# Performance work log

Hardware: AMD Instinct MI355X
Metric: run time of the kernel (lower is better)

## Reference

```python
import jax, jax.numpy as jnp
import numpy as np

N, E, G = 50000, 400000, 64
F_IN, HID, HEADS, GF, NCLS = 16, 128, 4, 10, 6


def _init(k, shape, fan):
    return jax.random.normal(k, shape, jnp.float32) * (1.0 / np.sqrt(fan))


def setup_inputs() -> dict:
    key = jax.random.key(0)
    ks = jax.random.split(key, 16)
    x = jax.random.normal(ks[0], (N, F_IN), jnp.float32)
    edge_index = jax.random.randint(ks[1], (2, E), 0, N)
    batch = jnp.sort(jax.random.randint(ks[2], (N,), 0, G))
    graph_feat = jax.random.normal(ks[3], (G, GF), jnp.float32)
    # GATConv 1: in=16 -> heads=4, out=128, concat
    W1 = _init(ks[4], (F_IN, HEADS * HID), F_IN)
    att_src1 = _init(ks[5], (HEADS, HID), HID)
    att_dst1 = _init(ks[6], (HEADS, HID), HID)
    b1 = jnp.zeros((HEADS * HID,), jnp.float32)
    # GATConv 2: in=512 -> heads=1, out=128, mean (concat=False)
    W2 = _init(ks[7], (HEADS * HID, HID), HEADS * HID)
    att_src2 = _init(ks[8], (1, HID), HID)
    att_dst2 = _init(ks[9], (1, HID), HID)
    b2 = jnp.zeros((HID,), jnp.float32)
    # graph_proj MLP 10->32->32
    Wg1 = _init(ks[10], (GF, 32), GF); bg1 = jnp.zeros((32,), jnp.float32)
    Wg2 = _init(ks[11], (32, 32), 32); bg2 = jnp.zeros((32,), jnp.float32)
    # classifier 160->128->6
    Wc1 = _init(ks[12], (HID + 32, 128), HID + 32); bc1 = jnp.zeros((128,), jnp.float32)
    Wc2 = _init(ks[13], (128, NCLS), 128); bc2 = jnp.zeros((NCLS,), jnp.float32)
    return dict(x=x, edge_index=edge_index, batch=batch, graph_feat=graph_feat,
                W1=W1, att_src1=att_src1, att_dst1=att_dst1, b1=b1,
                W2=W2, att_src2=att_src2, att_dst2=att_dst2, b2=b2,
                Wg1=Wg1, bg1=bg1, Wg2=Wg2, bg2=bg2,
                Wc1=Wc1, bc1=bc1, Wc2=Wc2, bc2=bc2)


def gat_layer(x, W, att_src, att_dst, bias, src, dst, n_nodes, heads, out_dim, concat):
    # Linear transform: [N, H, C]
    h = (x @ W).reshape(n_nodes, heads, out_dim)
    a_src = jnp.einsum('nhc,hc->nh', h, att_src)  # [N,H]
    a_dst = jnp.einsum('nhc,hc->nh', h, att_dst)  # [N,H]
    e = jax.nn.leaky_relu(a_src[src] + a_dst[dst], 0.2)  # [Etot,H]
    # segment softmax over edges grouped by dst (self-loops ensure nonempty)
    m = jax.ops.segment_max(e, dst, num_segments=n_nodes)
    ex = jnp.exp(e - m[dst])
    denom = jax.ops.segment_sum(ex, dst, num_segments=n_nodes)
    alpha = ex / denom[dst]  # [Etot,H]
    out = jax.ops.segment_sum(alpha[:, :, None] * h[src], dst, num_segments=n_nodes)  # [N,H,C]
    if concat:
        out = out.reshape(n_nodes, heads * out_dim)
    else:
        out = out.mean(axis=1)
    return out + bias


def reference(x, edge_index, batch, graph_feat,
              W1, att_src1, att_dst1, b1,
              W2, att_src2, att_dst2, b2,
              Wg1, bg1, Wg2, bg2, Wc1, bc1, Wc2, bc2):
    n = x.shape[0]
    loops = jnp.arange(n, dtype=edge_index.dtype)
    src = jnp.concatenate([edge_index[0], loops])
    dst = jnp.concatenate([edge_index[1], loops])
    h = jax.nn.elu(gat_layer(x, W1, att_src1, att_dst1, b1, src, dst, n, HEADS, HID, True))
    h = jax.nn.elu(gat_layer(h, W2, att_src2, att_dst2, b2, src, dst, n, 1, HID, False))
    # global mean pool over graphs
    g = graph_feat.shape[0]
    sums = jax.ops.segment_sum(h, batch, num_segments=g)
    counts = jax.ops.segment_sum(jnp.ones((n, 1), h.dtype), batch, num_segments=g)
    pooled = sums / jnp.maximum(counts, 1.0)
    gf = jax.nn.relu(graph_feat @ Wg1 + bg1) @ Wg2 + bg2
    z = jnp.concatenate([pooled, gf], axis=1)
    z = jax.nn.relu(z @ Wc1 + bc1)
    return z @ Wc2 + bc2
```

## Files before the change

kernel.cpp:

```cpp
#include <hip/hip_runtime.h>
#include <hip/hip_bf16.h>

#define NN 50000
#define EE 400000
#define GG 64
#define CAP 48

typedef unsigned short u16;
typedef unsigned char u8;
typedef long long i64;
typedef __attribute__((ext_vector_type(8))) short bf16x8;
typedef __attribute__((ext_vector_type(4))) float f32x4;
typedef __attribute__((ext_vector_type(2))) float f32x2;

__device__ __forceinline__ float b2f(u16 u) {
    unsigned int x = ((unsigned int)u) << 16;
    return __uint_as_float(x);
}
__device__ __forceinline__ u16 f2b(float f) {
    unsigned int x = __float_as_uint(f);
    unsigned int r = x + 0x7fffu + ((x >> 16) & 1u);
    return (u16)(r >> 16);
}
__device__ __forceinline__ u8 f2fp8(float f) {
    return (u8)(__builtin_amdgcn_cvt_pk_fp8_f32(f, f, 0, false) & 0xFF);
}
__device__ __forceinline__ f32x2 fp8x2_f32(unsigned int v, bool hi) {
    return hi ? __builtin_amdgcn_cvt_pk_f32_fp8(v, true)
              : __builtin_amdgcn_cvt_pk_f32_fp8(v, false);
}
__device__ __forceinline__ float wred_sum(float v) {
    #pragma unroll
    for (int o = 32; o; o >>= 1) v += __shfl_xor(v, o, 64);
    return v;
}
__device__ __forceinline__ float lrelu(float v) { return v > 0.f ? v : 0.2f * v; }

__global__ void k_prep(const int* __restrict__ batch, int* __restrict__ deg,
                       int* __restrict__ col, int* __restrict__ gstart,
                       const float* __restrict__ W1, const float* __restrict__ as1,
                       const float* __restrict__ ad1, u16* __restrict__ W1p,
                       const float* __restrict__ W2, u8* __restrict__ W2p,
                       float* __restrict__ pooled) {
    __shared__ float asw[16][8];
    int b = blockIdx.x, t = threadIdx.x;
    if (b < 196) {
        int n = b * 256 + t;
        if (n < NN) { deg[n] = 1; col[(size_t)n * CAP] = n; }
    } else if (b == 196) {
        if (t <= GG) {
            int lo = 0, hi = NN;
            while (lo < hi) {
                int mid = (lo + hi) >> 1;
                if (batch[mid] < t) lo = mid + 1; else hi = mid;
            }
            gstart[t] = lo;
        }
    } else if (b < 453) {
        int idx = (b - 197) * 256 + t;
        int j = idx & 7;
        int l = (idx >> 3) & 63;
        int ct = idx >> 9;
        int c = ct >> 3, tt = ct & 7;
        int k = c * 32 + (l >> 4) * 8 + j;
        int n = tt * 16 + (l & 15);
        W2p[idx] = f2fp8(W2[k * 128 + n]);
    } else if (b == 453) {
        int pair = t >> 1, half = t & 1;
        int k = pair >> 3, h = pair & 7;
        int hd = h & 3;
        const float* att = (h >= 4) ? ad1 : as1;
        float s = 0.f;
        int c0 = half * 64;
        for (int c = c0; c < c0 + 64; c++)
            s += W1[k * 512 + hd * 128 + c] * att[hd * 128 + c];
        s += __shfl_xor(s, 1, 64);
        if (half == 0) asw[k][h] = s;
        __syncthreads();
        for (int idx = t; idx < 33 * 64 * 8; idx += 256) {
            int j = idx & 7, l = (idx >> 3) & 63, tt = idx >> 9;
            int quad = l >> 4, m = l & 15;
            int k2 = quad * 8 + j;
            float v = 0.f;
            if (k2 < 16) {
                if (tt < 32) v = W1[k2 * 512 + tt * 16 + m];
                else if (m < 8) v = asw[k2][m];
            }
            W1p[idx] = f2b(v);
        }
    } else {
        for (int i = t; i < GG * 128; i += 256) pooled[i] = 0.f;
    }
}

__global__ void k_edges(const int* __restrict__ ei, int* __restrict__ deg,
                        int* __restrict__ col) {
    int e = blockIdx.x * 256 + threadIdx.x;
    if (e < EE) {
        int s = ei[e];
        int d = ei[EE + e];
        int slot = atomicAdd(&deg[d], 1);
        if (slot < CAP) col[(size_t)d * CAP + slot] = s;
    }
}

__global__ __launch_bounds__(256) void k_gemm1(
    const float* __restrict__ x, const u16* __restrict__ W1p,
    u8* __restrict__ h1, float* __restrict__ a_src1, float* __restrict__ a_dst1) {
    int tid = threadIdx.x;
    int wave = tid >> 6, l = tid & 63;
    int quad = l >> 4, m = l & 15;
    int row0 = blockIdx.x * 64 + wave * 16;
    int arow = row0 + m;
    int arow_c = arow < NN ? arow : (NN - 1);
    bf16x8 af;
    if (quad < 2) {
        const float* xp = x + arow_c * 16 + quad * 8;
        float4 x0 = *(const float4*)(xp);
        float4 x1 = *(const float4*)(xp + 4);
        u16 tmp[8] = {f2b(x0.x), f2b(x0.y), f2b(x0.z), f2b(x0.w),
                      f2b(x1.x), f2b(x1.y), f2b(x1.z), f2b(x1.w)};
        af = *(bf16x8*)tmp;
    } else {
        af = (bf16x8){0, 0, 0, 0, 0, 0, 0, 0};
    }
    const u16* bp = W1p + l * 8;
    f32x4 acc[33];
    #pragma unroll
    for (int tt = 0; tt < 33; tt++) acc[tt] = (f32x4){0.f, 0.f, 0.f, 0.f};
    #pragma unroll
    for (int tt = 0; tt < 33; tt++) {
        bf16x8 bf = *(const bf16x8*)(bp + (size_t)tt * 512);
        acc[tt] = __builtin_amdgcn_mfma_f32_16x16x32_bf16(af, bf, acc[tt], 0, 0, 0);
    }
    #pragma unroll
    for (int r = 0; r < 4; r++) {
        int row = row0 + quad * 4 + r;
        if (row >= NN) continue;
        #pragma unroll
        for (int tt = 0; tt < 32; tt++)
            h1[(size_t)row * 512 + tt * 16 + m] = f2fp8(acc[tt][r]);
        float v = acc[32][r];
        if (m < 4) a_src1[row * 4 + m] = v;
        else if (m < 8) a_dst1[row * 4 + (m - 4)] = v;
    }
}

__global__ __launch_bounds__(256) void k_agg1(
    const int* __restrict__ deg, const int* __restrict__ col,
    const float* __restrict__ a_src1, const float* __restrict__ a_dst1,
    const u8* __restrict__ h1, const float* __restrict__ b1,
    u8* __restrict__ h2pre) {
    __shared__ float alphaS[4][64][4];
    int t = threadIdx.x;
    int wave = t >> 6, l = t & 63;
    int n = blockIdx.x * 4 + wave;
    if (n >= NN) return;
    int dg = min(deg[n], CAP);
    int sl = (l < dg) ? col[(size_t)n * CAP + l] : 0;
    float4 ad = *(const float4*)(a_dst1 + n * 4);
    float4 as = *(const float4*)(a_src1 + (size_t)sl * 4);
    float4 e;
    e.x = __expf(lrelu(as.x + ad.x)); e.y = __expf(lrelu(as.y + ad.y));
    e.z = __expf(lrelu(as.z + ad.z)); e.w = __expf(lrelu(as.w + ad.w));
    if (l >= dg) e = (float4){0.f, 0.f, 0.f, 0.f};
    float4 inv;
    inv.x = 1.0f / wred_sum(e.x);
    inv.y = 1.0f / wred_sum(e.y);
    inv.z = 1.0f / wred_sum(e.z);
    inv.w = 1.0f / wred_sum(e.w);
    {
        float4 a4;
        a4.x = e.x * inv.x; a4.y = e.y * inv.y;
        a4.z = e.z * inv.z; a4.w = e.w * inv.w;
        *(float4*)&alphaS[wave][l][0] = a4;
    }
    int h = l >> 4;
    const u8* hb = h1 + l * 8;
    f32x2 acc[4] = {{0.f, 0.f}, {0.f, 0.f}, {0.f, 0.f}, {0.f, 0.f}};
    int iters = (dg + 3) >> 2;
    for (int j = 0; j < iters; j++) {
        int e0 = 4 * j, e1 = 4 * j + 1, e2 = 4 * j + 2, e3 = 4 * j + 3;
        int s0 = __shfl(sl, e0), s1 = __shfl(sl, e1);
        int s2 = __shfl(sl, e2), s3 = __shfl(sl, e3);
        float a0 = alphaS[wave][e0][h], a1 = alphaS[wave][e1][h];
        float a2 = alphaS[wave][e2][h], a3 = alphaS[wave][e3][h];
        uint2 u0 = *(const uint2*)(hb + (size_t)s0 * 512);
        uint2 u1 = *(const uint2*)(hb + (size_t)s1 * 512);
        uint2 u2 = *(const uint2*)(hb + (size_t)s2 * 512);
        uint2 u3 = *(const uint2*)(hb + (size_t)s3 * 512);
        acc[0] += a0 * fp8x2_f32(u0.x, false);
        acc[1] += a0 * fp8x2_f32(u0.x, true);
        acc[2] += a0 * fp8x2_f32(u0.y, false);
        acc[3] += a0 * fp8x2_f32(u0.y, true);
        acc[0] += a1 * fp8x2_f32(u1.x, false);
        acc[1] += a1 * fp8x2_f32(u1.x, true);
        acc[2] += a1 * fp8x2_f32(u1.y, false);
        acc[3] += a1 * fp8x2_f32(u1.y, true);
        acc[0] += a2 * fp8x2_f32(u2.x, false);
        acc[1] += a2 * fp8x2_f32(u2.x, true);
        acc[2] += a2 * fp8x2_f32(u2.y, false);
        acc[3] += a2 * fp8x2_f32(u2.y, true);
        acc[0] += a3 * fp8x2_f32(u3.x, false);
        acc[1] += a3 * fp8x2_f32(u3.x, true);
        acc[2] += a3 * fp8x2_f32(u3.y, false);
        acc[3] += a3 * fp8x2_f32(u3.y, true);
    }
    int ch0 = l * 8;
    float4 bA = *(const float4*)(b1 + ch0);
    float4 bB = *(const float4*)(b1 + ch0 + 4);
    float av[8] = {acc[0].x, acc[0].y, acc[1].x, acc[1].y,
                   acc[2].x, acc[2].y, acc[3].x, acc[3].y};
    float bb[8] = {bA.x, bA.y, bA.z, bA.w, bB.x, bB.y, bB.z, bB.w};
    float v[8];
    #pragma unroll
    for (int k = 0; k < 8; k++) {
        float w = av[k] + bb[k];
        v[k] = w > 0.f ? w : __expf(w) - 1.0f;
    }
    unsigned int d0 = __builtin_amdgcn_cvt_pk_fp8_f32(v[0], v[1], 0, false);
    d0 = __builtin_amdgcn_cvt_pk_fp8_f32(v[2], v[3], d0, true);
    unsigned int d1 = __builtin_amdgcn_cvt_pk_fp8_f32(v[4], v[5], 0, false);
    d1 = __builtin_amdgcn_cvt_pk_fp8_f32(v[6], v[7], d1, true);
    uint2 ov; ov.x = d0; ov.y = d1;
    *(uint2*)(h2pre + (size_t)n * 512 + ch0) = ov;
}

__global__ __launch_bounds__(256) void k_gemm2(
    const u8* __restrict__ h2pre, const u8* __restrict__ W2p,
    const float* __restrict__ as2, const float* __restrict__ ad2,
    u8* __restrict__ hL2, float* __restrict__ a_src2, float* __restrict__ a_dst2) {
    int t = threadIdx.x;
    int wave = t >> 6, l = t & 63;
    int quad = l >> 4, m = l & 15;
    int row0 = blockIdx.x * 64 + wave * 16;
    int arow = row0 + m;
    int arow_c = arow < NN ? arow : (NN - 1);
    const u8* aptr = h2pre + (size_t)arow_c * 512 + quad * 8;
    const u8* bptr = W2p + l * 8;
    f32x4 acc[8];
    #pragma unroll
    for (int tt = 0; tt < 8; tt++) acc[tt] = (f32x4){0.f, 0.f, 0.f, 0.f};
    for (int c = 0; c < 16; c++) {
        i64 af = *(const i64*)(aptr + c * 32);
        #pragma unroll
        for (int tt = 0; tt < 8; tt++) {
            i64 bf = *(const i64*)(bptr + (size_t)(c * 8 + tt) * 512);
            acc[tt] = __builtin_amdgcn_mfma_f32_16x16x32_fp8_fp8(af, bf, acc[tt], 0, 0, 0);
        }
    }
    float asv[8], adv[8];
    #pragma unroll
    for (int tt = 0; tt < 8; tt++) {
        int colc = tt * 16 + m;
        asv[tt] = as2[colc];
        adv[tt] = ad2[colc];
    }
    #pragma unroll
    for (int r = 0; r < 4; r++) {
        int row = row0 + quad * 4 + r;
        bool ok = row < NN;
        float rs = 0.f, rd = 0.f;
        #pragma unroll
        for (int tt = 0; tt < 8; tt++) {
            float v = acc[tt][r];
            if (ok) hL2[(size_t)row * 128 + tt * 16 + m] = f2fp8(v);
            rs += v * asv[tt];
            rd += v * adv[tt];
        }
        #pragma unroll
        for (int o = 1; o < 16; o <<= 1) {
            rs += __shfl_xor(rs, o, 64);
            rd += __shfl_xor(rd, o, 64);
        }
        if (ok && m == 0) { a_src2[row] = rs; a_dst2[row] = rd; }
    }
}

__global__ __launch_bounds__(256) void k_agg2(
    const int* __restrict__ deg, const int* __restrict__ col,
    const float* __restrict__ a_src2, const float* __restrict__ a_dst2,
    const u8* __restrict__ hL2, const float* __restrict__ b2v,
    const int* __restrict__ batch, float* __restrict__ pooled) {
    __shared__ float red[4][128];
    __shared__ int gS[4];
    int t = threadIdx.x;
    int wave = t >> 6, l = t & 63;
    int n = blockIdx.x * 4 + wave;
    if (n >= NN) return;
    int dg = min(deg[n], CAP);
    int sl = (l < dg) ? col[(size_t)n * CAP + l] : 0;
    float ad = a_dst2[n];
    float e = (l < dg) ? __expf(lrelu(a_src2[sl] + ad)) : 0.f;
    float inv = 1.0f / wred_sum(e);
    float al = e * inv;
    f32x2 acc = {0.f, 0.f};
    const u8* hb = hL2 + l * 2;
    int iters = (dg + 3) >> 2;
    for (int j = 0; j < iters; j++) {
        int e0 = 4 * j, e1 = 4 * j + 1, e2 = 4 * j + 2, e3 = 4 * j + 3;
        int s0 = __shfl(sl, e0), s1 = __shfl(sl, e1);
        int s2 = __shfl(sl, e2), s3 = __shfl(sl, e3);
        float a0 = __shfl(al, e0), a1 = __shfl(al, e1);
        float a2 = __shfl(al, e2), a3 = __shfl(al, e3);
        unsigned int u0 = *(const u16*)(hb + (size_t)s0 * 128);
        unsigned int u1 = *(const u16*)(hb + (size_t)s1 * 128);
        unsigned int u2 = *(const u16*)(hb + (size_t)s2 * 128);
        unsigned int u3 = *(const u16*)(hb + (size_t)s3 * 128);
        acc += a0 * fp8x2_f32(u0, false);
        acc += a1 * fp8x2_f32(u1, false);
        acc += a2 * fp8x2_f32(u2, false);
        acc += a3 * fp8x2_f32(u3, false);
    }
    float o0 = acc.x + b2v[2 * l];     o0 = o0 > 0.f ? o0 : __expf(o0) - 1.0f;
    float o1 = acc.y + b2v[2 * l + 1]; o1 = o1 > 0.f ? o1 : __expf(o1) - 1.0f;
    red[wave][2 * l] = o0;
    red[wave][2 * l + 1] = o1;
    if (l == 0) gS[wave] = batch[n];
    __syncthreads();
    if (t < 128) {
        int g0 = gS[0];
        if (gS[1] == g0 && gS[2] == g0 && gS[3] == g0) {
            float s = red[0][t] + red[1][t] + red[2][t] + red[3][t];
            atomicAdd(&pooled[g0 * 128 + t], s);
        } else {
            #pragma unroll
            for (int w = 0; w < 4; w++)
                atomicAdd(&pooled[gS[w] * 128 + t], red[w][t]);
        }
    }
}

__global__ __launch_bounds__(128) void k_head(
    const int* __restrict__ gstart, const float* __restrict__ pooled,
    const float* __restrict__ gfeat,
    const float* __restrict__ Wg1, const float* __restrict__ bg1,
    const float* __restrict__ Wg2, const float* __restrict__ bg2,
    const float* __restrict__ Wc1, const float* __restrict__ bc1,
    const float* __restrict__ Wc2, const float* __restrict__ bc2,
    float* __restrict__ out) {
    __shared__ float z[160];
    __shared__ float hg[32];
    __shared__ float c1b[128];
    int g = blockIdx.x, t = threadIdx.x;
    float cntf = (float)(gstart[g + 1] - gstart[g]);
    z[t] = pooled[g * 128 + t] / fmaxf(cntf, 1.0f);
    if (t < 32) {
        float a = bg1[t];
        for (int i = 0; i < 10; i++) a += gfeat[g * 10 + i] * Wg1[i * 32 + t];
        hg[t] = fmaxf(a, 0.f);
    }
    __syncthreads();
    if (t < 32) {
        float a = bg2[t];
        for (int i = 0; i < 32; i++) a += hg[i] * Wg2[i * 32 + t];
        z[128 + t] = a;
    }
    __syncthreads();
    float a = bc1[t];
    for (int i = 0; i < 160; i++) a += z[i] * Wc1[i * 128 + t];
    c1b[t] = fmaxf(a, 0.f);
    __syncthreads();
    if (t < 6) {
        float o = bc2[t];
        for (int i = 0; i < 128; i++) o += c1b[i] * Wc2[i * 6 + t];
        out[g * 6 + t] = o;
    }
}

extern "C" void kernel_launch(void* const* d_in, const int* in_sizes, int n_in,
                              void* d_out, int out_size, void* d_ws, size_t ws_size,
                              hipStream_t stream) {
    const float* x     = (const float*)d_in[0];
    const int*   ei    = (const int*)d_in[1];
    const int*   batch = (const int*)d_in[2];
    const float* gfeat = (const float*)d_in[3];
    const float* W1    = (const float*)d_in[4];
    const float* as1   = (const float*)d_in[5];
    const float* ad1   = (const float*)d_in[6];
    const float* b1    = (const float*)d_in[7];
    const float* W2    = (const float*)d_in[8];
    const float* as2   = (const float*)d_in[9];
    const float* ad2   = (const float*)d_in[10];
    const float* b2    = (const float*)d_in[11];
    const float* Wg1   = (const float*)d_in[12];
    const float* bg1   = (const float*)d_in[13];
    const float* Wg2   = (const float*)d_in[14];
    const float* bg2   = (const float*)d_in[15];
    const float* Wc1   = (const float*)d_in[16];
    const float* bc1   = (const float*)d_in[17];
    const float* Wc2   = (const float*)d_in[18];
    const float* bc2   = (const float*)d_in[19];
    float* out = (float*)d_out;

    size_t off = 0;
    char* base = (char*)d_ws;
    auto take = [&](size_t nbytes) -> char* {
        char* p = base + off;
        off = (off + nbytes + 255) & ~(size_t)255;
        return p;
    };
    u8*    h1     = (u8*)take((size_t)NN * 512);
    u8*    h2pre  = (u8*)take((size_t)NN * 512);
    u8*    hL2    = (u8*)take((size_t)NN * 128);
    float* a_src1 = (float*)take((size_t)NN * 4 * 4);
    float* a_dst1 = (float*)take((size_t)NN * 4 * 4);
    float* a_src2 = (float*)take((size_t)NN * 4);
    float* a_dst2 = (float*)take((size_t)NN * 4);
    int*   deg    = (int*)take((size_t)NN * 4);
    int*   col    = (int*)take((size_t)NN * CAP * 4);
    float* pooled = (float*)take(GG * 128 * 4);
    int*   gstart = (int*)take((GG + 1) * 4);
    u8*    W2p    = (u8*)take((size_t)512 * 128);
    u16*   W1p    = (u16*)take((size_t)33 * 64 * 8 * 2);
    (void)ws_size; (void)in_sizes; (void)n_in; (void)out_size;

    k_prep<<<455, 256, 0, stream>>>(batch, deg, col, gstart, W1, as1, ad1, W1p,
                                    W2, W2p, pooled);
    k_edges<<<(EE + 255) / 256, 256, 0, stream>>>(ei, deg, col);
    k_gemm1<<<(NN + 63) / 64, 256, 0, stream>>>(x, W1p, h1, a_src1, a_dst1);
    k_agg1<<<(NN + 3) / 4, 256, 0, stream>>>(deg, col, a_src1, a_dst1, h1, b1, h2pre);
    k_gemm2<<<(NN + 63) / 64, 256, 0, stream>>>(h2pre, W2p, as2, ad2, hL2, a_src2, a_dst2);
    k_agg2<<<(NN + 3) / 4, 256, 0, stream>>>(deg, col, a_src2, a_dst2, hL2, b2,
                                             batch, pooled);
    k_head<<<GG, 128, 0, stream>>>(gstart, pooled, gfeat, Wg1, bg1, Wg2, bg2,
                                   Wc1, bc1, Wc2, bc2, out);
}
```

Measured before the change: 256.6 us.

## Merge edge-bucketing into GEMM1 launch and permute h1 layout for vector stores

Merges the edge CSR-bucketing kernel into the first GEMM kernel as extra blocks, so one launch serves both and the two independent jobs can overlap. It also changes the h1 channel layout so each GEMM lane packs 32 fp8 values and writes them with two 16-byte stores instead of 32 single-byte stores. The aggregation kernel reads with the matching permuted offsets and writes its output channels as strided single bytes. The risk is that those byte writes in the aggregation kernel are less efficient than the previous 8-byte store.

```diff
diff --git a/kernel.cpp b/kernel.cpp
--- a/kernel.cpp
+++ b/kernel.cpp
@@ -5,6 +5,7 @@
 #define EE 400000
 #define GG 64
 #define CAP 48
+#define GB1 782
 
 typedef unsigned short u16;
 typedef unsigned char u8;
@@ -93,21 +94,21 @@
     }
 }
 
-__global__ void k_edges(const int* __restrict__ ei, int* __restrict__ deg,
-                        int* __restrict__ col) {
-    int e = blockIdx.x * 256 + threadIdx.x;
-    if (e < EE) {
-        int s = ei[e];
-        int d = ei[EE + e];
-        int slot = atomicAdd(&deg[d], 1);
-        if (slot < CAP) col[(size_t)d * CAP + slot] = s;
-    }
-}
-
-__global__ __launch_bounds__(256) void k_gemm1(
+__global__ __launch_bounds__(256) void k_ge(
     const float* __restrict__ x, const u16* __restrict__ W1p,
-    u8* __restrict__ h1, float* __restrict__ a_src1, float* __restrict__ a_dst1) {
+    u8* __restrict__ h1, float* __restrict__ a_src1, float* __restrict__ a_dst1,
+    const int* __restrict__ ei, int* __restrict__ deg, int* __restrict__ col) {
     int tid = threadIdx.x;
+    if (blockIdx.x >= GB1) {
+        int e = (blockIdx.x - GB1) * 256 + tid;
+        if (e < EE) {
+            int s = ei[e];
+            int d = ei[EE + e];
+            int slot = atomicAdd(&deg[d], 1);
+            if (slot < CAP) col[(size_t)d * CAP + slot] = s;
+        }
+        return;
+    }
     int wave = tid >> 6, l = tid & 63;
     int quad = l >> 4, m = l & 15;
     int row0 = blockIdx.x * 64 + wave * 16;
@@ -137,9 +138,17 @@
     for (int r = 0; r < 4; r++) {
         int row = row0 + quad * 4 + r;
         if (row >= NN) continue;
+        unsigned int d[8];
         #pragma unroll
-        for (int tt = 0; tt < 32; tt++)
-            h1[(size_t)row * 512 + tt * 16 + m] = f2fp8(acc[tt][r]);
+        for (int dd = 0; dd < 8; dd++) {
+            unsigned int w = __builtin_amdgcn_cvt_pk_fp8_f32(acc[4 * dd][r], acc[4 * dd + 1][r], 0, false);
+            w = __builtin_amdgcn_cvt_pk_fp8_f32(acc[4 * dd + 2][r], acc[4 * dd + 3][r], w, true);
+            d[dd] = w;
+        }
+        uint4 v0; v0.x = d[0]; v0.y = d[1]; v0.z = d[2]; v0.w = d[3];
+        uint4 v1; v1.x = d[4]; v1.y = d[5]; v1.z = d[6]; v1.w = d[7];
+        *(uint4*)(h1 + (size_t)row * 512 + m * 32) = v0;
+        *(uint4*)(h1 + (size_t)row * 512 + m * 32 + 16) = v1;
         float v = acc[32][r];
         if (m < 4) a_src1[row * 4 + m] = v;
         else if (m < 8) a_dst1[row * 4 + (m - 4)] = v;
@@ -175,16 +184,16 @@
         a4.z = e.z * inv.z; a4.w = e.w * inv.w;
         *(float4*)&alphaS[wave][l][0] = a4;
     }
-    int h = l >> 4;
-    const u8* hb = h1 + l * 8;
+    int g = l >> 4, m = l & 15;
+    const u8* hb = h1 + m * 32 + g * 8;
     f32x2 acc[4] = {{0.f, 0.f}, {0.f, 0.f}, {0.f, 0.f}, {0.f, 0.f}};
     int iters = (dg + 3) >> 2;
     for (int j = 0; j < iters; j++) {
         int e0 = 4 * j, e1 = 4 * j + 1, e2 = 4 * j + 2, e3 = 4 * j + 3;
         int s0 = __shfl(sl, e0), s1 = __shfl(sl, e1);
         int s2 = __shfl(sl, e2), s3 = __shfl(sl, e3);
-        float a0 = alphaS[wave][e0][h], a1 = alphaS[wave][e1][h];
-        float a2 = alphaS[wave][e2][h], a3 = alphaS[wave][e3][h];
+        float a0 = alphaS[wave][e0][g], a1 = alphaS[wave][e1][g];
+        float a2 = alphaS[wave][e2][g], a3 = alphaS[wave][e3][g];
         uint2 u0 = *(const uint2*)(hb + (size_t)s0 * 512);
         uint2 u1 = *(const uint2*)(hb + (size_t)s1 * 512);
         uint2 u2 = *(const uint2*)(hb + (size_t)s2 * 512);
@@ -206,24 +215,16 @@
         acc[2] += a3 * fp8x2_f32(u3.y, false);
         acc[3] += a3 * fp8x2_f32(u3.y, true);
     }
-    int ch0 = l * 8;
-    float4 bA = *(const float4*)(b1 + ch0);
-    float4 bB = *(const float4*)(b1 + ch0 + 4);
     float av[8] = {acc[0].x, acc[0].y, acc[1].x, acc[1].y,
                    acc[2].x, acc[2].y, acc[3].x, acc[3].y};
-    float bb[8] = {bA.x, bA.y, bA.z, bA.w, bB.x, bB.y, bB.z, bB.w};
-    float v[8];
-    #pragma unroll
-    for (int k = 0; k < 8; k++) {
-        float w = av[k] + bb[k];
-        v[k] = w > 0.f ? w : __expf(w) - 1.0f;
-    }
-    unsigned int d0 = __builtin_amdgcn_cvt_pk_fp8_f32(v[0], v[1], 0, false);
-    d0 = __builtin_amdgcn_cvt_pk_fp8_f32(v[2], v[3], d0, true);
-    unsigned int d1 = __builtin_amdgcn_cvt_pk_fp8_f32(v[4], v[5], 0, false);
-    d1 = __builtin_amdgcn_cvt_pk_fp8_f32(v[6], v[7], d1, true);
-    uint2 ov; ov.x = d0; ov.y = d1;
-    *(uint2*)(h2pre + (size_t)n * 512 + ch0) = ov;
+    u8* op = h2pre + (size_t)n * 512 + 128 * g + m;
+    const float* bb = b1 + 128 * g + m;
+    #pragma unroll
+    for (int j = 0; j < 8; j++) {
+        float v = av[j] + bb[16 * j];
+        v = v > 0.f ? v : __expf(v) - 1.0f;
+        op[16 * j] = f2fp8(v);
+    }
 }
 
 __global__ __launch_bounds__(256) void k_gemm2(
@@ -417,8 +418,8 @@
 
     k_prep<<<455, 256, 0, stream>>>(batch, deg, col, gstart, W1, as1, ad1, W1p,
                                     W2, W2p, pooled);
-    k_edges<<<(EE + 255) / 256, 256, 0, stream>>>(ei, deg, col);
-    k_gemm1<<<(NN + 63) / 64, 256, 0, stream>>>(x, W1p, h1, a_src1, a_dst1);
+    k_ge<<<GB1 + (EE + 255) / 256, 256, 0, stream>>>(x, W1p, h1, a_src1, a_dst1,
+                                                     ei, deg, col);
     k_agg1<<<(NN + 3) / 4, 256, 0, stream>>>(deg, col, a_src1, a_dst1, h1, b1, h2pre);
     k_gemm2<<<(NN + 63) / 64, 256, 0, stream>>>(h2pre, W2p, as2, ad2, hL2, a_src2, a_dst2);
     k_agg2<<<(NN + 3) / 4, 256, 0, stream>>>(deg, col, a_src2, a_dst2, hL2, b2,
```

Measured after the change: 262.3 us. 2.2% more time.
